# Optimization experiments

Hardware: AMD Instinct MI355X
Metric: run time of the kernel (lower is better)

The kernel has to match this reference:

```python
import jax, jax.numpy as jnp
import numpy as np

B, S, D_IN, D_OUT = 4, 4096, 1024, 1024

def setup_inputs() -> dict:
    key = jax.random.key(0)
    kx, kq, kk, kv = jax.random.split(key, 4)
    x = jax.random.normal(kx, (B, S, D_IN), dtype=jnp.float32)
    # torch nn.Linear stores weight as [d_out, d_in]; y = x @ W.T
    Wq = jax.random.normal(kq, (D_OUT, D_IN), dtype=jnp.float32) * 0.02
    Wk = jax.random.normal(kk, (D_OUT, D_IN), dtype=jnp.float32) * 0.02
    Wv = jax.random.normal(kv, (D_OUT, D_IN), dtype=jnp.float32) * 0.02
    return {"x": x, "Wq": Wq, "Wk": Wk, "Wv": Wv}

def reference(x, Wq, Wk, Wv):
    b, n, _ = x.shape
    d_out = Wk.shape[0]
    q = jnp.einsum('bnd,od->bno', x, Wq)
    k = jnp.einsum('bnd,od->bno', x, Wk)
    v = jnp.einsum('bnd,od->bno', x, Wv)
    scores = jnp.einsum('bqo,bko->bqk', q, k)  # [B, S, S]
    causal = jnp.triu(jnp.ones((n, n), dtype=bool), k=1)
    scores = jnp.where(causal, -jnp.inf, scores)
    attn = jax.nn.softmax(scores / jnp.sqrt(jnp.float32(d_out)), axis=-1)
    # dropout p=0.0 -> identity
    return jnp.einsum('bqk,bko->bqo', attn, v)
```

## Files before the change

kernel.cpp:

```cpp
#include <hip/hip_runtime.h>


typedef unsigned short u16;
typedef unsigned int u32;
typedef __attribute__((ext_vector_type(8))) short bf16x8;
typedef __attribute__((ext_vector_type(4))) float f32x4;
typedef __attribute__((ext_vector_type(8))) unsigned short u16x8;

__device__ __forceinline__ u16 f2bf(float f) {
  union { float f; unsigned u; } v; v.f = f;
  unsigned r = v.u + 0x7FFFu + ((v.u >> 16) & 1u);
  return (u16)(r >> 16);
}
__device__ __forceinline__ float bf2f(u16 h) {
  union { unsigned u; float f; } v; v.u = ((unsigned)h) << 16;
  return v.f;
}
__device__ __forceinline__ f32x4 mfma16(bf16x8 a, bf16x8 b, f32x4 c) {
  return __builtin_amdgcn_mfma_f32_16x16x32_bf16(a, b, c, 0, 0, 0);
}
__device__ __forceinline__ void gld_lds16(const u16* g, u16* l) {
  __builtin_amdgcn_global_load_lds(
      (const __attribute__((address_space(1))) u32*)g,
      (__attribute__((address_space(3))) u32*)l, 16, 0, 0);
}

__global__ __launch_bounds__(256)
void cast_f32_bf16(const float* __restrict__ src, u16* __restrict__ dst, int n8) {
  int i = blockIdx.x * 256 + threadIdx.x;
  if (i >= n8) return;
  const float4* s4 = (const float4*)src;
  float4 a = s4[2*i], b = s4[2*i+1];
  u16x8 o;
  o[0]=f2bf(a.x); o[1]=f2bf(a.y); o[2]=f2bf(a.z); o[3]=f2bf(a.w);
  o[4]=f2bf(b.x); o[5]=f2bf(b.y); o[6]=f2bf(b.z); o[7]=f2bf(b.w);
  ((u16x8*)dst)[i] = o;
}

__global__ __launch_bounds__(512)
void qkv_gemm(const u16* __restrict__ X, const u16* __restrict__ W,
              u16* __restrict__ Qo, u16* __restrict__ Ko, u16* __restrict__ VTo) {
  __shared__ __align__(16) u16 At[2][256 * 64];
  __shared__ __align__(16) u16 Bt[2][256 * 64];
  const int tid = threadIdx.x;
  const int w = tid >> 6, lane = tid & 63;
  const int g = lane >> 4, c16 = lane & 15;
  const int wr = w >> 2, wc = w & 3;
  const int M0 = blockIdx.x * 256;
  const int N0 = blockIdx.y * 256;

  f32x4 acc[8][4] = {};

  auto stage = [&](int s, int k0) {
#pragma unroll
    for (int i = 0; i < 4; ++i) {
      int ci = i * 512 + tid;
      int r = ci >> 3;
      int c = (ci & 7) ^ (r & 7);
      gld_lds16(X + (size_t)(M0 + r) * 1024 + k0 + c * 8, &At[s][ci * 8]);
    }
#pragma unroll
    for (int i = 0; i < 4; ++i) {
      int ci = i * 512 + tid;
      int r = ci >> 3;
      int c = (ci & 7) ^ (r & 7);
      gld_lds16(W + (size_t)(N0 + r) * 1024 + k0 + c * 8, &Bt[s][ci * 8]);
    }
  };
  auto compute = [&](int s) {
#pragma unroll
    for (int dk = 0; dk < 2; ++dk) {
      bf16x8 af[8], bfr[4];
#pragma unroll
      for (int m = 0; m < 8; ++m) {
        int row = wr * 128 + m * 16 + c16;
        int ch = dk * 4 + g;
        af[m] = *(const bf16x8*)&At[s][row * 64 + ((ch ^ (row & 7)) * 8)];
      }
#pragma unroll
      for (int n = 0; n < 4; ++n) {
        int row = wc * 64 + n * 16 + c16;
        int ch = dk * 4 + g;
        bfr[n] = *(const bf16x8*)&Bt[s][row * 64 + ((ch ^ (row & 7)) * 8)];
      }
#pragma unroll
      for (int m = 0; m < 8; ++m)
#pragma unroll
        for (int n = 0; n < 4; ++n)
          acc[m][n] = mfma16(af[m], bfr[n], acc[m][n]);
    }
  };

  stage(0, 0);
  __syncthreads();
  int cur = 0;
  for (int t = 0; t < 16; ++t) {
    if (t < 15) stage(cur ^ 1, (t + 1) * 64);
    compute(cur);
    __syncthreads();
    cur ^= 1;
  }

  const int which = N0 >> 10;
  const int colbase = N0 & 1023;
#pragma unroll
  for (int m = 0; m < 8; ++m) {
#pragma unroll
    for (int n = 0; n < 4; ++n) {
#pragma unroll
      for (int r = 0; r < 4; ++r) {
        int gm  = M0 + wr * 128 + m * 16 + 4 * g + r;
        int col = colbase + wc * 64 + n * 16 + c16;
        u16 hv = f2bf(acc[m][n][r]);
        if (which == 0) {
          Qo[(size_t)gm * 1024 + col] = hv;
        } else if (which == 1) {
          Ko[(size_t)gm * 1024 + col] = hv;
        } else {
          int b = gm >> 12, s = gm & 4095;
          VTo[((size_t)((b << 10) + col)) * 4096 + s] = hv;
        }
      }
    }
  }
}

__global__ __launch_bounds__(512)
void sgemm_exp(const u16* __restrict__ Q, const u16* __restrict__ K,
               u16* __restrict__ Spack, float* __restrict__ lpart) {
  __shared__ __align__(16) u16 At[2][256 * 64];
  __shared__ __align__(16) u16 Bt[2][256 * 64];
  __shared__ float lsum[256][4];
  const int tid = threadIdx.x;
  const int w = tid >> 6, lane = tid & 63;
  const int g = lane >> 4, c16 = lane & 15;
  const int wr = w >> 2, wc = w & 3;
  const int b = blockIdx.y;

  int L = blockIdx.x, qt = 0;
  while ((qt + 1) * (qt + 2) / 2 <= L) ++qt;
  const int kt = L - qt * (qt + 1) / 2;

  const u16* Qb = Q + (size_t)b * 4096 * 1024 + (size_t)qt * 256 * 1024;
  const u16* Kb = K + (size_t)b * 4096 * 1024 + (size_t)kt * 256 * 1024;

  f32x4 acc[8][4] = {};

  auto stage = [&](int s, int k0) {
#pragma unroll
    for (int i = 0; i < 4; ++i) {
      int ci = i * 512 + tid;
      int r = ci >> 3;
      int c = (ci & 7) ^ (r & 7);
      gld_lds16(Qb + (size_t)r * 1024 + k0 + c * 8, &At[s][ci * 8]);
    }
#pragma unroll
    for (int i = 0; i < 4; ++i) {
      int ci = i * 512 + tid;
      int r = ci >> 3;
      int c = (ci & 7) ^ (r & 7);
      gld_lds16(Kb + (size_t)r * 1024 + k0 + c * 8, &Bt[s][ci * 8]);
    }
  };
  auto compute = [&](int s) {
#pragma unroll
    for (int dk = 0; dk < 2; ++dk) {
      bf16x8 af[8], bfr[4];
#pragma unroll
      for (int m = 0; m < 8; ++m) {
        int row = wr * 128 + m * 16 + c16;
        int ch = dk * 4 + g;
        af[m] = *(const bf16x8*)&At[s][row * 64 + ((ch ^ (row & 7)) * 8)];
      }
#pragma unroll
      for (int n = 0; n < 4; ++n) {
        int row = wc * 64 + n * 16 + c16;
        int ch = dk * 4 + g;
        bfr[n] = *(const bf16x8*)&Bt[s][row * 64 + ((ch ^ (row & 7)) * 8)];
      }
#pragma unroll
      for (int m = 0; m < 8; ++m)
#pragma unroll
        for (int n = 0; n < 4; ++n)
          acc[m][n] = mfma16(af[m], bfr[n], acc[m][n]);
    }
  };

  stage(0, 0);
  __syncthreads();
  int cur = 0;
  for (int t = 0; t < 16; ++t) {
    if (t < 15) stage(cur ^ 1, (t + 1) * 64);
    compute(cur);
    __syncthreads();
    cur ^= 1;
  }

  const int qt128 = 2 * qt + wr;
  const int kt128 = 2 * kt + (wc >> 1);
  const bool exists = (kt128 <= qt128);
  u16* Sb = Spack + (((size_t)b * 528 + (size_t)(qt128 * (qt128 + 1)) / 2 + kt128) << 14);
  const int q0 = qt * 256, k0g = kt * 256;
  float psum[8][4];
#pragma unroll
  for (int m = 0; m < 8; ++m)
#pragma unroll
    for (int r = 0; r < 4; ++r) psum[m][r] = 0.f;
#pragma unroll
  for (int m = 0; m < 8; ++m) {
#pragma unroll
    for (int n = 0; n < 4; ++n) {
#pragma unroll
      for (int r = 0; r < 4; ++r) {
        int rl = wr * 128 + m * 16 + 4 * g + r;
        int cl = wc * 64 + n * 16 + c16;
        float s = acc[m][n][r] * 0.03125f;
        float p = (k0g + cl <= q0 + rl) ? __expf(s) : 0.f;
        u16 pb = f2bf(p);
        if (exists) Sb[(rl & 127) * 128 + (cl & 127)] = pb;
        psum[m][r] += bf2f(pb);
      }
    }
  }
#pragma unroll
  for (int m = 0; m < 8; ++m)
#pragma unroll
    for (int r = 0; r < 4; ++r) {
      float v = psum[m][r];
      v += __shfl_xor(v, 1, 64);
      v += __shfl_xor(v, 2, 64);
      v += __shfl_xor(v, 4, 64);
      v += __shfl_xor(v, 8, 64);
      psum[m][r] = v;
    }
  if (c16 == 0) {
#pragma unroll
    for (int m = 0; m < 8; ++m)
#pragma unroll
      for (int r = 0; r < 4; ++r)
        lsum[wr * 128 + m * 16 + 4 * g + r][wc] = psum[m][r];
  }
  __syncthreads();
  if (tid < 256) {
    float v = lsum[tid][0] + lsum[tid][1] + lsum[tid][2] + lsum[tid][3];
    lpart[((size_t)b * 4096 + q0 + tid) * 16 + kt] = v;
  }
}

__global__ __launch_bounds__(256)
void lreduce(const float* __restrict__ lpart, float* __restrict__ linv) {
  int row = blockIdx.x * 256 + threadIdx.x;
  int nt  = ((row & 4095) >> 8) + 1;
  const float* p = lpart + (size_t)row * 16;
  float s = 0.f;
  for (int i = 0; i < nt; ++i) s += p[i];
  linv[row] = 1.f / s;
}

__global__ __launch_bounds__(512)
void pv_gemm(const u16* __restrict__ Spack, const u16* __restrict__ VT,
             const u16* __restrict__ ztile, const float* __restrict__ linv,
             float* __restrict__ Out) {
  __shared__ __align__(16) u16 At[2][256 * 64];
  __shared__ __align__(16) u16 Bt[2][128 * 64];
  const int tid = threadIdx.x;
  const int w = tid >> 6, lane = tid & 63;
  const int g = lane >> 4, c16 = lane & 15;
  const int wm = w >> 1, wn = w & 1;
  const int p  = blockIdx.x;
  const int d0 = blockIdx.y;
  const int b  = blockIdx.z;

  const u16* Sp_b = Spack + (size_t)b * 528 * 16384;
  const u16* VTb  = VT + (size_t)b * 1024 * 4096;
  float* Ob = Out + (size_t)b * 4096 * 1024;

  for (int pass = 0; pass < 2; ++pass) {
    const int QT = pass == 0 ? p : 15 - p;
    const int M0 = QT * 256;
    const int nsteps = (QT + 1) * 4;
    const int tLo = 2 * QT;
    const size_t triLo = (size_t)(tLo * (tLo + 1)) / 2;
    const size_t triHi = (size_t)((tLo + 1) * (tLo + 2)) / 2;

    f32x4 acc[4][4] = {};

    auto stage = [&](int s, int tt) {
      const int kv0 = tt * 64;
      const int kt128 = tt >> 1;
      const int koff = (tt & 1) * 64;
      const u16* baseLo = (kt128 <= tLo) ? Sp_b + ((triLo + kt128) << 14) : ztile;
      const u16* baseHi = Sp_b + ((triHi + kt128) << 14);
#pragma unroll
      for (int i = 0; i < 4; ++i) {
        int ci = i * 512 + tid;
        int r = ci >> 3;
        int c = (ci & 7) ^ (r & 7);
        const u16* base = (i < 2) ? baseLo : baseHi;
        gld_lds16(base + (size_t)(r & 127) * 128 + koff + c * 8, &At[s][ci * 8]);
      }
#pragma unroll
      for (int i = 0; i < 2; ++i) {
        int ci = i * 512 + tid;
        int r = ci >> 3;
        int c = (ci & 7) ^ (r & 7);
        gld_lds16(VTb + (size_t)(d0 * 128 + r) * 4096 + kv0 + c * 8, &Bt[s][ci * 8]);
      }
    };
    auto compute = [&](int s) {
#pragma unroll
      for (int dk = 0; dk < 2; ++dk) {
        bf16x8 af[4], bfr[4];
#pragma unroll
        for (int m = 0; m < 4; ++m) {
          int row = wm * 64 + m * 16 + c16;
          int ch = dk * 4 + g;
          af[m] = *(const bf16x8*)&At[s][row * 64 + ((ch ^ (row & 7)) * 8)];
        }
#pragma unroll
        for (int n = 0; n < 4; ++n) {
          int row = wn * 64 + n * 16 + c16;
          int ch = dk * 4 + g;
          bfr[n] = *(const bf16x8*)&Bt[s][row * 64 + ((ch ^ (row & 7)) * 8)];
        }
#pragma unroll
        for (int m = 0; m < 4; ++m)
#pragma unroll
          for (int n = 0; n < 4; ++n)
            acc[m][n] = mfma16(af[m], bfr[n], acc[m][n]);
      }
    };

    stage(0, 0);
    __syncthreads();
    int cur = 0;
    for (int t = 0; t < nsteps; ++t) {
      if (t + 1 < nsteps) stage(cur ^ 1, t + 1);
      compute(cur);
      __syncthreads();
      cur ^= 1;
    }

    const float* lb = linv + (size_t)b * 4096 + M0;
#pragma unroll
    for (int m = 0; m < 4; ++m) {
#pragma unroll
      for (int r = 0; r < 4; ++r) {
        int rl = wm * 64 + m * 16 + 4 * g + r;
        float li = lb[rl];
#pragma unroll
        for (int n = 0; n < 4; ++n) {
          int dcol = d0 * 128 + wn * 64 + n * 16 + c16;
          Ob[(size_t)(M0 + rl) * 1024 + dcol] = acc[m][n][r] * li;
        }
      }
    }
  }
}

__global__ __launch_bounds__(512, 2)
void attn_kernel(const u16* __restrict__ Q, const u16* __restrict__ K,
                 const u16* __restrict__ VT, float* __restrict__ Out) {
  __shared__ u16 kv_lds[32 * 1024];
  __shared__ float s_part[4][32][33];
  __shared__ u16 p_lds[32 * 40];
  __shared__ float l_lds[32];

  const int tid = threadIdx.x;
  const int w = tid >> 6, lane = tid & 63;
  const int g = lane >> 4, c16 = lane & 15;
  const int b  = blockIdx.x & 3;
  const int qb = 127 - (blockIdx.x >> 2);
  const int qs = qb * 32;
  const int kh = w & 1, dq = w >> 1;

  const u16* Qb  = Q  + (size_t)b * 4096 * 1024;
  const u16* Kb  = K  + (size_t)b * 4096 * 1024;
  const u16* VTb = VT + (size_t)b * 1024 * 4096;

  bf16x8 qfrag[2][8];
#pragma unroll
  for (int qh = 0; qh < 2; ++qh)
#pragma unroll
    for (int dk = 0; dk < 8; ++dk)
      qfrag[qh][dk] = *(const bf16x8*)(Qb + (size_t)(qs + qh * 16 + c16) * 1024
                                       + dq * 256 + dk * 32 + g * 8);

  f32x4 oacc[2][8] = {};
  if (tid < 32) l_lds[tid] = 0.f;

  const int qrow_p = tid >> 4;
  const int kk     = tid & 15;
  const int gq     = qs + qrow_p;

  for (int j = 0; j <= qb; ++j) {
    const int kv0 = j * 32;
    __syncthreads();
    uint4 rk[8];
#pragma unroll
    for (int i = 0; i < 8; ++i) {
      int ci = i * 512 + tid;
      int r  = ci >> 7;
      int c  = (ci & 127) ^ (r & 7);
      rk[i] = *(const uint4*)(Kb + (size_t)(kv0 + r) * 1024 + c * 8);
    }
#pragma unroll
    for (int i = 0; i < 8; ++i)
      *(uint4*)&kv_lds[(size_t)(i * 512 + tid) * 8] = rk[i];
    __syncthreads();
    f32x4 sacc[2] = {};
#pragma unroll
    for (int dk = 0; dk < 8; ++dk) {
      int kvrow = kh * 16 + c16;
      int ch    = dq * 32 + dk * 4 + g;
      bf16x8 kf = *(const bf16x8*)&kv_lds[kvrow * 1024 + ((ch ^ (kvrow & 7)) * 8)];
      sacc[0] = mfma16(qfrag[0][dk], kf, sacc[0]);
      sacc[1] = mfma16(qfrag[1][dk], kf, sacc[1]);
    }
#pragma unroll
    for (int qh = 0; qh < 2; ++qh)
#pragma unroll
      for (int r = 0; r < 4; ++r)
        s_part[dq][qh * 16 + 4 * g + r][kh * 16 + c16] = sacc[qh][r];
    __syncthreads();
    uint4 rv[8];
#pragma unroll
    for (int i = 0; i < 8; ++i) {
      int ci = i * 512 + tid;
      int d  = ((ci >> 6) << 4) + (ci & 15);
      int c  = (ci >> 4) & 3;
      rv[i] = *(const uint4*)(VTb + (size_t)d * 4096 + kv0 + c * 8);
    }
    {
      float psum = 0.f;
#pragma unroll
      for (int h = 0; h < 2; ++h) {
        int kcol = kk + h * 16;
        float s = s_part[0][qrow_p][kcol] + s_part[1][qrow_p][kcol]
                + s_part[2][qrow_p][kcol] + s_part[3][qrow_p][kcol];
        s *= 0.03125f;
        float p = (kv0 + kcol <= gq) ? __expf(s) : 0.f;
        u16 pb = f2bf(p);
        p_lds[qrow_p * 40 + kcol] = pb;
        psum += bf2f(pb);
      }
#pragma unroll
      for (int off = 1; off < 16; off <<= 1)
        psum += __shfl_xor(psum, off, 64);
      if (kk == 0) l_lds[qrow_p] += psum;
    }
#pragma unroll
    for (int i = 0; i < 8; ++i)
      *(uint4*)&kv_lds[(size_t)(i * 512 + tid) * 8] = rv[i];
    __syncthreads();
    bf16x8 pa0 = *(const bf16x8*)&p_lds[(0  + c16) * 40 + g * 8];
    bf16x8 pa1 = *(const bf16x8*)&p_lds[(16 + c16) * 40 + g * 8];
#pragma unroll
    for (int f = 0; f < 8; ++f) {
      int dcol = w * 128 + f * 16 + c16;
      int pos  = (dcol >> 4) * 64 + g * 16 + (dcol & 15);
      bf16x8 vf = *(const bf16x8*)&kv_lds[(size_t)pos * 8];
      oacc[0][f] = mfma16(pa0, vf, oacc[0][f]);
      oacc[1][f] = mfma16(pa1, vf, oacc[1][f]);
    }
  }

  float* Ob = Out + (size_t)b * 4096 * 1024;
#pragma unroll
  for (int qh = 0; qh < 2; ++qh) {
#pragma unroll
    for (int r = 0; r < 4; ++r) {
      int ql = qh * 16 + 4 * g + r;
      float linvv = 1.f / l_lds[ql];
#pragma unroll
      for (int f = 0; f < 8; ++f)
        Ob[(size_t)(qs + ql) * 1024 + w * 128 + f * 16 + c16] = oacc[qh][f][r] * linvv;
    }
  }
}

extern "C" void kernel_launch(void* const* d_in, const int* in_sizes, int n_in,
                              void* d_out, int out_size, void* d_ws, size_t ws_size,
                              hipStream_t stream) {
  const float* x  = (const float*)d_in[0];
  const float* Wq = (const float*)d_in[1];
  const float* Wk = (const float*)d_in[2];
  const float* Wv = (const float*)d_in[3];
  float* out = (float*)d_out;

  u16* ws    = (u16*)d_ws;
  u16* wWqkv = ws;
  u16* wX    = wWqkv + (size_t)3 * 1024 * 1024;
  u16* wQ    = wX + (size_t)16384 * 1024;
  u16* wK    = wQ + (size_t)16384 * 1024;
  u16* wVT   = wK + (size_t)16384 * 1024;
  u16* wSp   = wVT + (size_t)16384 * 1024;
  float* lpart = (float*)(ws + (size_t)104857600);
  float* linv  = (float*)(ws + (size_t)105906176);

  cast_f32_bf16<<<dim3(8192), 256, 0, stream>>>(x, wX, 16777216 / 8);
  cast_f32_bf16<<<dim3(512), 256, 0, stream>>>(Wq, wWqkv,                 1048576 / 8);
  cast_f32_bf16<<<dim3(512), 256, 0, stream>>>(Wk, wWqkv + 1048576,       1048576 / 8);
  cast_f32_bf16<<<dim3(512), 256, 0, stream>>>(Wv, wWqkv + 2 * 1048576,   1048576 / 8);

  qkv_gemm<<<dim3(64, 12), 512, 0, stream>>>(wX, wWqkv, wQ, wK, wVT);

  if (ws_size >= (size_t)211877888) {
    hipMemsetAsync(wX, 0, 32768, stream);
    sgemm_exp<<<dim3(136, 4), 512, 0, stream>>>(wQ, wK, wSp, lpart);
    lreduce<<<dim3(64), 256, 0, stream>>>(lpart, linv);
    pv_gemm<<<dim3(8, 8, 4), 512, 0, stream>>>(wSp, wVT, wX, linv, out);
  } else {
    attn_kernel<<<dim3(512), 512, 0, stream>>>(wQ, wK, wVT, out);
  }
}
```

Baseline: 393.6 us.

## Merge cast launches, fold lreduce into pv_gemm, remap blocks across XCDs

The four f32-to-bf16 cast launches become one kernel that picks its source by index range. The row-sum reduction kernel is removed, and pv_gemm now computes inverse row sums into LDS at its start. qkv_gemm and sgemm_exp remap block IDs so consecutive blocks on the same XCD share M tiles or triangle regions, aiming for better L2 reuse. Together these cut launch overhead and one small kernel, in exchange for redundant row-sum work repeated across the 8 d0 blocks.

Result: faster. 373.4 us (-5.1%).

```diff
diff --git a/kernel.cpp b/kernel.cpp
--- a/kernel.cpp
+++ b/kernel.cpp
@@ -26,15 +26,22 @@
 }
 
 __global__ __launch_bounds__(256)
-void cast_f32_bf16(const float* __restrict__ src, u16* __restrict__ dst, int n8) {
+void cast_all(const float* __restrict__ x, const float* __restrict__ Wq,
+              const float* __restrict__ Wk, const float* __restrict__ Wv,
+              u16* __restrict__ wX, u16* __restrict__ wWqkv) {
   int i = blockIdx.x * 256 + threadIdx.x;
-  if (i >= n8) return;
+  const float* src; u16* dst; int j;
+  if (i < 2097152)        { src = x;  dst = wX;                j = i; }
+  else if (i < 2228224)   { src = Wq; dst = wWqkv;             j = i - 2097152; }
+  else if (i < 2359296)   { src = Wk; dst = wWqkv + 1048576;   j = i - 2228224; }
+  else if (i < 2490368)   { src = Wv; dst = wWqkv + 2097152;   j = i - 2359296; }
+  else return;
   const float4* s4 = (const float4*)src;
-  float4 a = s4[2*i], b = s4[2*i+1];
+  float4 a = s4[2*j], b = s4[2*j+1];
   u16x8 o;
   o[0]=f2bf(a.x); o[1]=f2bf(a.y); o[2]=f2bf(a.z); o[3]=f2bf(a.w);
   o[4]=f2bf(b.x); o[5]=f2bf(b.y); o[6]=f2bf(b.z); o[7]=f2bf(b.w);
-  ((u16x8*)dst)[i] = o;
+  ((u16x8*)dst)[j] = o;
 }
 
 __global__ __launch_bounds__(512)
@@ -46,8 +53,10 @@
   const int w = tid >> 6, lane = tid & 63;
   const int g = lane >> 4, c16 = lane & 15;
   const int wr = w >> 2, wc = w & 3;
-  const int M0 = blockIdx.x * 256;
-  const int N0 = blockIdx.y * 256;
+  const int lid = blockIdx.x;
+  const int xcd = lid & 7, gg = lid >> 3;
+  const int M0 = ((xcd << 3) | (gg & 7)) * 256;
+  const int N0 = (gg >> 3) * 256;
 
   f32x4 acc[8][4] = {};
 
@@ -137,7 +146,8 @@
   const int wr = w >> 2, wc = w & 3;
   const int b = blockIdx.y;
 
-  int L = blockIdx.x, qt = 0;
+  int L = (blockIdx.x & 7) * 17 + (blockIdx.x >> 3);
+  int qt = 0;
   while ((qt + 1) * (qt + 2) / 2 <= L) ++qt;
   const int kt = L - qt * (qt + 1) / 2;
 
@@ -247,27 +257,18 @@
   }
 }
 
-__global__ __launch_bounds__(256)
-void lreduce(const float* __restrict__ lpart, float* __restrict__ linv) {
-  int row = blockIdx.x * 256 + threadIdx.x;
-  int nt  = ((row & 4095) >> 8) + 1;
-  const float* p = lpart + (size_t)row * 16;
-  float s = 0.f;
-  for (int i = 0; i < nt; ++i) s += p[i];
-  linv[row] = 1.f / s;
-}
-
 __global__ __launch_bounds__(512)
 void pv_gemm(const u16* __restrict__ Spack, const u16* __restrict__ VT,
-             const u16* __restrict__ ztile, const float* __restrict__ linv,
+             const u16* __restrict__ ztile, const float* __restrict__ lpart,
              float* __restrict__ Out) {
   __shared__ __align__(16) u16 At[2][256 * 64];
   __shared__ __align__(16) u16 Bt[2][128 * 64];
+  __shared__ float linv_lds[512];
   const int tid = threadIdx.x;
   const int w = tid >> 6, lane = tid & 63;
   const int g = lane >> 4, c16 = lane & 15;
   const int wm = w >> 1, wn = w & 1;
-  const int p  = blockIdx.x;
+  const int pp = blockIdx.x;
   const int d0 = blockIdx.y;
   const int b  = blockIdx.z;
 
@@ -275,8 +276,18 @@
   const u16* VTb  = VT + (size_t)b * 1024 * 4096;
   float* Ob = Out + (size_t)b * 4096 * 1024;
 
+  {
+    const int QTr = (tid < 256) ? pp : (15 - pp);
+    const int row = QTr * 256 + (tid & 255);
+    const int nt  = QTr + 1;
+    const float* p = lpart + ((size_t)b * 4096 + row) * 16;
+    float s = 0.f;
+    for (int i = 0; i < nt; ++i) s += p[i];
+    linv_lds[tid] = 1.f / s;
+  }
+
   for (int pass = 0; pass < 2; ++pass) {
-    const int QT = pass == 0 ? p : 15 - p;
+    const int QT = pass == 0 ? pp : 15 - pp;
     const int M0 = QT * 256;
     const int nsteps = (QT + 1) * 4;
     const int tLo = 2 * QT;
@@ -341,7 +352,7 @@
       cur ^= 1;
     }
 
-    const float* lb = linv + (size_t)b * 4096 + M0;
+    const float* lb = linv_lds + pass * 256;
 #pragma unroll
     for (int m = 0; m < 4; ++m) {
 #pragma unroll
@@ -496,20 +507,15 @@
   u16* wVT   = wK + (size_t)16384 * 1024;
   u16* wSp   = wVT + (size_t)16384 * 1024;
   float* lpart = (float*)(ws + (size_t)104857600);
-  float* linv  = (float*)(ws + (size_t)105906176);
-
-  cast_f32_bf16<<<dim3(8192), 256, 0, stream>>>(x, wX, 16777216 / 8);
-  cast_f32_bf16<<<dim3(512), 256, 0, stream>>>(Wq, wWqkv,                 1048576 / 8);
-  cast_f32_bf16<<<dim3(512), 256, 0, stream>>>(Wk, wWqkv + 1048576,       1048576 / 8);
-  cast_f32_bf16<<<dim3(512), 256, 0, stream>>>(Wv, wWqkv + 2 * 1048576,   1048576 / 8);
-
-  qkv_gemm<<<dim3(64, 12), 512, 0, stream>>>(wX, wWqkv, wQ, wK, wVT);
+
+  cast_all<<<dim3(9728), 256, 0, stream>>>(x, Wq, Wk, Wv, wX, wWqkv);
+
+  qkv_gemm<<<dim3(768), 512, 0, stream>>>(wX, wWqkv, wQ, wK, wVT);
 
   if (ws_size >= (size_t)211877888) {
     hipMemsetAsync(wX, 0, 32768, stream);
     sgemm_exp<<<dim3(136, 4), 512, 0, stream>>>(wQ, wK, wSp, lpart);
-    lreduce<<<dim3(64), 256, 0, stream>>>(lpart, linv);
-    pv_gemm<<<dim3(8, 8, 4), 512, 0, stream>>>(wSp, wVT, wX, linv, out);
+    pv_gemm<<<dim3(8, 8, 4), 512, 0, stream>>>(wSp, wVT, wX, lpart, out);
   } else {
     attn_kernel<<<dim3(512), 512, 0, stream>>>(wQ, wK, wVT, out);
   }
```
